# Kernel optimization log

Hardware: AMD Instinct MI355X
Metric: run time of the kernel (lower is better)

The kernel has to match this reference:

```python
import jax, jax.numpy as jnp
import numpy as np

E, T, A, H = 64, 128, 32, 4
S, O, QH1, QD, C1 = 256, 128, 128, 64, 128  # state, obs, query hidden, query/key dim, c hidden


def setup_inputs() -> dict:
    key = jax.random.key(0)
    ks = jax.random.split(key, 10)
    w = 0.02
    return {
        "q_values": jax.random.normal(ks[0], (E, T, A), jnp.float32),
        "states": jax.random.normal(ks[1], (E, T, S), jnp.float32),
        "individual_fs": jax.random.normal(ks[2], (E, T, A, O), jnp.float32),
        "Wq1": jax.random.normal(ks[3], (S, QH1), jnp.float32) * w,
        "bq1": jnp.zeros((QH1,), jnp.float32),
        "Wq2": jax.random.normal(ks[4], (QH1, QD), jnp.float32) * w,
        "bq2": jnp.zeros((QD,), jnp.float32),
        "Wk": jax.random.normal(ks[5], (H, O, QD), jnp.float32) * w,
        "bk": jnp.zeros((H, QD), jnp.float32),
        "Wc1": jax.random.normal(ks[6], (S, C1), jnp.float32) * w,
        "bc1": jnp.zeros((C1,), jnp.float32),
        "Wc2": jax.random.normal(ks[7], (C1, 1), jnp.float32) * w,
        "bc2": jnp.zeros((1,), jnp.float32),
    }


def reference(q_values, states, individual_fs, Wq1, bq1, Wq2, bq2, Wk, bk, Wc1, bc1, Wc2, bc2):
    e, t, a = q_values.shape
    s = states.reshape(-1, states.shape[-1])              # (B, S), B = E*T
    f = individual_fs.reshape(e * t, a, -1)               # (B, A, O)
    # query embedding of state: 2-layer MLP with ReLU
    emb_s = jnp.maximum(s @ Wq1 + bq1, 0.0) @ Wq2 + bq2   # (B, QD)
    # all-agents, all-heads key extraction in one batched einsum
    emb_u = jnp.einsum('bao,hok->bahk', f, Wk) + bk       # (B, A, H, QD)
    # query-key dot products per agent/head, then sum over heads
    Lambda_i = jnp.einsum('bk,bahk->bah', emb_s, emb_u).sum(axis=-1)  # (B, A)
    # state-dependent scalar bias
    c_value = jnp.maximum(s @ Wc1 + bc1, 0.0) @ Wc2 + bc2  # (B, 1)
    Q_tot = jnp.sum(Lambda_i * q_values.reshape(-1, a), axis=-1, keepdims=True) + c_value
    return Q_tot.reshape(e, t, 1)
```

## Files before the change

kernel.cpp:

```cpp
#include <hip/hip_runtime.h>


static constexpr int Sd  = 256;
static constexpr int Ad  = 32;
static constexpr int Od  = 128;
static constexpr int QDd = 64;

static constexpr size_t WS_WKT   = 0;
static constexpr size_t WS_BKSUM = 8192;
static constexpr size_t WS_M     = 8256;
static constexpr size_t WS_V0    = 24640;
static constexpr size_t WS_MBETA = 24768;
static constexpr size_t WS_BETA0 = 24896;
static constexpr size_t WS_BIAS  = 24960;
static constexpr size_t WS_V     = 33216;

__global__ void qatten_prep1(const float* __restrict__ Wk, const float* __restrict__ bk,
                             float* __restrict__ WkT, float* __restrict__ bkSum)
{
    int idx = blockIdx.x * 256 + threadIdx.x;
    int k = idx >> 7;
    int o = idx & 127;
    float s = 0.f;
#pragma unroll
    for (int h = 0; h < 4; ++h) s += Wk[h * (Od * QDd) + o * QDd + k];
    WkT[k * Od + o] = s;
    if (idx < QDd) {
        float t = 0.f;
#pragma unroll
        for (int h = 0; h < 4; ++h) t += bk[h * QDd + idx];
        bkSum[idx] = t;
    }
}

__global__ void qatten_prep2(const float* __restrict__ Wq2, const float* __restrict__ bq2,
                             const float* __restrict__ WkT, const float* __restrict__ bkSum,
                             float* __restrict__ M, float* __restrict__ v0,
                             float* __restrict__ m_beta, float* __restrict__ beta0)
{
    int idx = blockIdx.x * 256 + threadIdx.x;
    int j = idx >> 7;
    int o = idx & 127;
    float acc = 0.f;
    for (int k = 0; k < QDd; ++k)
        acc = fmaf(Wq2[j * QDd + k], WkT[k * Od + o], acc);
    M[j * Od + o] = acc;
    if (idx < 128) {
        float a = 0.f;
        for (int k = 0; k < QDd; ++k) a = fmaf(bq2[k], WkT[k * Od + idx], a);
        v0[idx] = a;
    } else if (idx < 256) {
        const int jj = idx - 128;
        float a = 0.f;
        for (int k = 0; k < QDd; ++k) a = fmaf(Wq2[jj * QDd + k], bkSum[k], a);
        m_beta[jj] = a;
    }
    if (idx == 0) {
        float a = 0.f;
        for (int k = 0; k < QDd; ++k) a = fmaf(bq2[k], bkSum[k], a);
        beta0[0] = a;
    }
}

static constexpr int NBM = 16;

__global__ __launch_bounds__(256, 4) void qatten_mlp(
    const float* __restrict__ qv, const float* __restrict__ st,
    const float* __restrict__ Wq1, const float* __restrict__ bq1,
    const float* __restrict__ Wc1, const float* __restrict__ bc1,
    const float* __restrict__ Wc2, const float* __restrict__ bc2,
    const float* __restrict__ M, const float* __restrict__ v0,
    const float* __restrict__ m_beta, const float* __restrict__ beta0p,
    float* __restrict__ v_ws, float* __restrict__ bias_ws)
{
    __shared__ float s_lds[NBM][Sd];
    __shared__ float h_lds[NBM][258];
    __shared__ float q_lds[NBM][Ad];

    const int tid = threadIdx.x;
    const int b0 = blockIdx.x * NBM;

    {
        const float4* sp = (const float4*)(st + (size_t)b0 * Sd);
        float4* sl = (float4*)&s_lds[0][0];
#pragma unroll
        for (int i = 0; i < 4; ++i) sl[tid + i * 256] = sp[tid + i * 256];
        float* ql = &q_lds[0][0];
#pragma unroll
        for (int i = 0; i < 2; ++i) ql[tid + i * 256] = qv[(size_t)b0 * Ad + tid + i * 256];
    }
    __syncthreads();

    {
        const float* W  = (tid < 128) ? (Wq1 + tid) : (Wc1 + (tid - 128));
        const float  bb = (tid < 128) ? bq1[tid] : bc1[tid - 128];
        float acc[NBM];
#pragma unroll
        for (int r = 0; r < NBM; ++r) acc[r] = 0.f;
        for (int i = 0; i < Sd; i += 4) {
            const float w0 = W[(size_t)(i + 0) * 128];
            const float w1 = W[(size_t)(i + 1) * 128];
            const float w2 = W[(size_t)(i + 2) * 128];
            const float w3 = W[(size_t)(i + 3) * 128];
#pragma unroll
            for (int r = 0; r < NBM; ++r) {
                const float4 sv = *(const float4*)&s_lds[r][i];
                float a = acc[r];
                a = fmaf(sv.x, w0, a);
                a = fmaf(sv.y, w1, a);
                a = fmaf(sv.z, w2, a);
                a = fmaf(sv.w, w3, a);
                acc[r] = a;
            }
        }
#pragma unroll
        for (int r = 0; r < NBM; ++r)
            h_lds[r][tid] = fmaxf(acc[r] + bb, 0.f);
    }
    __syncthreads();

    {
        const int o = tid & 127;
        const int rg = (tid >> 7) * 8;
        float acc[8];
#pragma unroll
        for (int r = 0; r < 8; ++r) acc[r] = 0.f;
        for (int j = 0; j < 128; j += 4) {
            const float m0 = M[(size_t)(j + 0) * 128 + o];
            const float m1 = M[(size_t)(j + 1) * 128 + o];
            const float m2 = M[(size_t)(j + 2) * 128 + o];
            const float m3 = M[(size_t)(j + 3) * 128 + o];
#pragma unroll
            for (int r = 0; r < 8; ++r) {
                const float4 hv = *(const float4*)&h_lds[rg + r][j];
                float a = acc[r];
                a = fmaf(hv.x, m0, a);
                a = fmaf(hv.y, m1, a);
                a = fmaf(hv.z, m2, a);
                a = fmaf(hv.w, m3, a);
                acc[r] = a;
            }
        }
        const float v0o = v0[o];
#pragma unroll
        for (int r = 0; r < 8; ++r)
            v_ws[(size_t)(b0 + rg + r) * 128 + o] = acc[r] + v0o;
    }

    {
        const int b = tid >> 4;
        const int i = tid & 15;
        float pb = 0.f, pc = 0.f;
#pragma unroll
        for (int t = 0; t < 8; ++t) {
            const int j = i + 16 * t;
            pb = fmaf(h_lds[b][j], m_beta[j], pb);
            pc = fmaf(h_lds[b][128 + j], Wc2[j], pc);
        }
        float pq = q_lds[b][i] + q_lds[b][i + 16];
#pragma unroll
        for (int d = 8; d >= 1; d >>= 1) {
            pb += __shfl_down(pb, d, 16);
            pc += __shfl_down(pc, d, 16);
            pq += __shfl_down(pq, d, 16);
        }
        if (i == 0) bias_ws[b0 + b] = (pc + bc2[0]) + (pb + beta0p[0]) * pq;
    }
}

__global__ __launch_bounds__(256, 8) void qatten_stream(
    const float* __restrict__ qv, const float* __restrict__ fs,
    const float* __restrict__ v_ws, const float* __restrict__ bias_ws,
    float* __restrict__ out)
{
    const int gw   = (blockIdx.x * 256 + threadIdx.x) >> 6;
    const int lane = threadIdx.x & 63;
    const int oq   = lane & 31;
    const int a0   = lane >> 5;

    const float4* fb = (const float4*)(fs + (size_t)gw * (Ad * Od));
    const float4  v4 = *(const float4*)(v_ws + (size_t)gw * Od + oq * 4);
    const float*  qb = qv + (size_t)gw * Ad;

    float s = 0.f;
#pragma unroll
    for (int r = 0; r < 16; ++r) {
        const int a = a0 + 2 * r;
        const float4 f4 = fb[a * 32 + oq];
        float d = f4.x * v4.x;
        d = fmaf(f4.y, v4.y, d);
        d = fmaf(f4.z, v4.z, d);
        d = fmaf(f4.w, v4.w, d);
        s = fmaf(qb[a], d, s);
    }
#pragma unroll
    for (int d = 32; d >= 1; d >>= 1) s += __shfl_xor(s, d);
    if (lane == 0) out[gw] = s + bias_ws[gw];
}

extern "C" void kernel_launch(void* const* d_in, const int* in_sizes, int n_in,
                              void* d_out, int out_size, void* d_ws, size_t ws_size,
                              hipStream_t stream) {
    const float* qv  = (const float*)d_in[0];
    const float* st  = (const float*)d_in[1];
    const float* fs  = (const float*)d_in[2];
    const float* Wq1 = (const float*)d_in[3];
    const float* bq1 = (const float*)d_in[4];
    const float* Wq2 = (const float*)d_in[5];
    const float* bq2 = (const float*)d_in[6];
    const float* Wk  = (const float*)d_in[7];
    const float* bk  = (const float*)d_in[8];
    const float* Wc1 = (const float*)d_in[9];
    const float* bc1 = (const float*)d_in[10];
    const float* Wc2 = (const float*)d_in[11];
    const float* bc2 = (const float*)d_in[12];
    float* out = (float*)d_out;

    float* ws      = (float*)d_ws;
    float* WkT     = ws + WS_WKT;
    float* bkSum   = ws + WS_BKSUM;
    float* Mm      = ws + WS_M;
    float* v0      = ws + WS_V0;
    float* m_beta  = ws + WS_MBETA;
    float* beta0   = ws + WS_BETA0;
    float* bias_ws = ws + WS_BIAS;
    float* v_ws    = ws + WS_V;

    qatten_prep1<<<32, 256, 0, stream>>>(Wk, bk, WkT, bkSum);
    qatten_prep2<<<64, 256, 0, stream>>>(Wq2, bq2, WkT, bkSum, Mm, v0, m_beta, beta0);
    qatten_mlp<<<512, 256, 0, stream>>>(qv, st, Wq1, bq1, Wc1, bc1, Wc2, bc2,
                                        Mm, v0, m_beta, beta0, v_ws, bias_ws);
    qatten_stream<<<2048, 256, 0, stream>>>(qv, fs, v_ws, bias_ws, out);
}
```

Baseline: 268.7 us.

## Fuse MLP and feature-stream kernels with register prefetch of individual_fs

Merges the per-row MLP kernel and the streaming dot-product kernel into one kernel handling 8 rows per block, so the intermediate v and bias stay in LDS instead of a global workspace. The first 6 rows' individual_fs tiles are prefetched into registers before and during the MLP stages to overlap the dominant 33MB read with compute. It also replaces __syncthreads with a custom LDS-only waitcnt barrier. In exchange, row batching drops from 16 to 8, so weights are re-read twice as often, and the many prefetch registers may reduce occupancy.

```diff
diff --git a/kernel.cpp b/kernel.cpp
--- a/kernel.cpp
+++ b/kernel.cpp
@@ -5,6 +5,7 @@
 static constexpr int Ad  = 32;
 static constexpr int Od  = 128;
 static constexpr int QDd = 64;
+static constexpr int NB  = 8;
 
 static constexpr size_t WS_WKT   = 0;
 static constexpr size_t WS_BKSUM = 8192;
@@ -12,8 +13,13 @@
 static constexpr size_t WS_V0    = 24640;
 static constexpr size_t WS_MBETA = 24768;
 static constexpr size_t WS_BETA0 = 24896;
-static constexpr size_t WS_BIAS  = 24960;
-static constexpr size_t WS_V     = 33216;
+
+__device__ __forceinline__ void barrier_lds() {
+    asm volatile("" ::: "memory");
+    __builtin_amdgcn_s_waitcnt(0xc07f);
+    __builtin_amdgcn_s_barrier();
+    asm volatile("" ::: "memory");
+}
 
 __global__ void qatten_prep1(const float* __restrict__ Wk, const float* __restrict__ bk,
                              float* __restrict__ WkT, float* __restrict__ bkSum)
@@ -62,76 +68,88 @@
     }
 }
 
-static constexpr int NBM = 16;
-
-__global__ __launch_bounds__(256, 4) void qatten_mlp(
-    const float* __restrict__ qv, const float* __restrict__ st,
+__global__ __launch_bounds__(256, 4) void qatten_fused(
+    const float* __restrict__ qv, const float* __restrict__ st, const float* __restrict__ fs,
     const float* __restrict__ Wq1, const float* __restrict__ bq1,
     const float* __restrict__ Wc1, const float* __restrict__ bc1,
     const float* __restrict__ Wc2, const float* __restrict__ bc2,
     const float* __restrict__ M, const float* __restrict__ v0,
     const float* __restrict__ m_beta, const float* __restrict__ beta0p,
-    float* __restrict__ v_ws, float* __restrict__ bias_ws)
+    float* __restrict__ out)
 {
-    __shared__ float s_lds[NBM][Sd];
-    __shared__ float h_lds[NBM][258];
-    __shared__ float q_lds[NBM][Ad];
+    __shared__ float s_lds[NB][Sd];
+    __shared__ float h_lds[NB][258];
+    __shared__ float v_lds[NB][Od];
+    __shared__ float q_lds[NB][Ad];
+    __shared__ float red_lds[NB][4];
+    __shared__ float bias_lds[NB];
 
     const int tid = threadIdx.x;
-    const int b0 = blockIdx.x * NBM;
-
-    {
-        const float4* sp = (const float4*)(st + (size_t)b0 * Sd);
-        float4* sl = (float4*)&s_lds[0][0];
-#pragma unroll
-        for (int i = 0; i < 4; ++i) sl[tid + i * 256] = sp[tid + i * 256];
-        float* ql = &q_lds[0][0];
-#pragma unroll
-        for (int i = 0; i < 2; ++i) ql[tid + i * 256] = qv[(size_t)b0 * Ad + tid + i * 256];
-    }
-    __syncthreads();
+    const int b0 = blockIdx.x * NB;
+    const int oq = tid & 31;
+    const int ag = tid >> 5;
+
+    const float4* sp = (const float4*)(st + (size_t)b0 * Sd);
+    const float4 sstage0 = sp[tid];
+    const float4 sstage1 = sp[tid + 256];
+    const float  qstage  = qv[(size_t)b0 * Ad + tid];
+
+    const float4* fbase = (const float4*)(fs + (size_t)b0 * (Ad * Od));
+    float4 pf[16];
+#pragma unroll
+    for (int b = 0; b < 4; ++b)
+#pragma unroll
+        for (int r = 0; r < 4; ++r)
+            pf[b * 4 + r] = fbase[(size_t)b * 1024 + (ag + 8 * r) * 32 + oq];
+
+    ((float4*)&s_lds[0][0])[tid]       = sstage0;
+    ((float4*)&s_lds[0][0])[tid + 256] = sstage1;
+    (&q_lds[0][0])[tid] = qstage;
+    barrier_lds();
 
     {
         const float* W  = (tid < 128) ? (Wq1 + tid) : (Wc1 + (tid - 128));
         const float  bb = (tid < 128) ? bq1[tid] : bc1[tid - 128];
-        float acc[NBM];
-#pragma unroll
-        for (int r = 0; r < NBM; ++r) acc[r] = 0.f;
-        for (int i = 0; i < Sd; i += 4) {
-            const float w0 = W[(size_t)(i + 0) * 128];
-            const float w1 = W[(size_t)(i + 1) * 128];
-            const float w2 = W[(size_t)(i + 2) * 128];
-            const float w3 = W[(size_t)(i + 3) * 128];
-#pragma unroll
-            for (int r = 0; r < NBM; ++r) {
-                const float4 sv = *(const float4*)&s_lds[r][i];
+        float acc[NB];
+#pragma unroll
+        for (int r = 0; r < NB; ++r) acc[r] = 0.f;
+        for (int i = 0; i < Sd; i += 8) {
+            float w[8];
+#pragma unroll
+            for (int u = 0; u < 8; ++u) w[u] = W[(size_t)(i + u) * 128];
+#pragma unroll
+            for (int r = 0; r < NB; ++r) {
+                const float4 s0 = *(const float4*)&s_lds[r][i];
+                const float4 s1 = *(const float4*)&s_lds[r][i + 4];
                 float a = acc[r];
-                a = fmaf(sv.x, w0, a);
-                a = fmaf(sv.y, w1, a);
-                a = fmaf(sv.z, w2, a);
-                a = fmaf(sv.w, w3, a);
+                a = fmaf(s0.x, w[0], a);
+                a = fmaf(s0.y, w[1], a);
+                a = fmaf(s0.z, w[2], a);
+                a = fmaf(s0.w, w[3], a);
+                a = fmaf(s1.x, w[4], a);
+                a = fmaf(s1.y, w[5], a);
+                a = fmaf(s1.z, w[6], a);
+                a = fmaf(s1.w, w[7], a);
                 acc[r] = a;
             }
         }
 #pragma unroll
-        for (int r = 0; r < NBM; ++r)
+        for (int r = 0; r < NB; ++r)
             h_lds[r][tid] = fmaxf(acc[r] + bb, 0.f);
     }
-    __syncthreads();
+    barrier_lds();
 
     {
         const int o = tid & 127;
-        const int rg = (tid >> 7) * 8;
-        float acc[8];
-#pragma unroll
-        for (int r = 0; r < 8; ++r) acc[r] = 0.f;
+        const int rg = (tid >> 7) * 4;
+        float acc[4] = {0.f, 0.f, 0.f, 0.f};
         for (int j = 0; j < 128; j += 4) {
             const float m0 = M[(size_t)(j + 0) * 128 + o];
             const float m1 = M[(size_t)(j + 1) * 128 + o];
             const float m2 = M[(size_t)(j + 2) * 128 + o];
             const float m3 = M[(size_t)(j + 3) * 128 + o];
 #pragma unroll
-            for (int r = 0; r < 8; ++r) {
+            for (int r = 0; r < 4; ++r) {
                 const float4 hv = *(const float4*)&h_lds[rg + r][j];
                 float a = acc[r];
                 a = fmaf(hv.x, m0, a);
@@ -143,59 +161,105 @@
         }
         const float v0o = v0[o];
 #pragma unroll
-        for (int r = 0; r < 8; ++r)
-            v_ws[(size_t)(b0 + rg + r) * 128 + o] = acc[r] + v0o;
-    }
-
-    {
-        const int b = tid >> 4;
-        const int i = tid & 15;
+        for (int r = 0; r < 4; ++r) v_lds[rg + r][o] = acc[r] + v0o;
+    }
+
+    float4 pf2[8];
+#pragma unroll
+    for (int b = 0; b < 2; ++b)
+#pragma unroll
+        for (int r = 0; r < 4; ++r)
+            pf2[b * 4 + r] = fbase[(size_t)(4 + b) * 1024 + (ag + 8 * r) * 32 + oq];
+
+    {
+        const int b = tid >> 5;
+        const int i = tid & 31;
         float pb = 0.f, pc = 0.f;
 #pragma unroll
-        for (int t = 0; t < 8; ++t) {
-            const int j = i + 16 * t;
+        for (int t = 0; t < 4; ++t) {
+            const int j = i + 32 * t;
             pb = fmaf(h_lds[b][j], m_beta[j], pb);
             pc = fmaf(h_lds[b][128 + j], Wc2[j], pc);
         }
-        float pq = q_lds[b][i] + q_lds[b][i + 16];
-#pragma unroll
-        for (int d = 8; d >= 1; d >>= 1) {
-            pb += __shfl_down(pb, d, 16);
-            pc += __shfl_down(pc, d, 16);
-            pq += __shfl_down(pq, d, 16);
-        }
-        if (i == 0) bias_ws[b0 + b] = (pc + bc2[0]) + (pb + beta0p[0]) * pq;
-    }
-}
-
-__global__ __launch_bounds__(256, 8) void qatten_stream(
-    const float* __restrict__ qv, const float* __restrict__ fs,
-    const float* __restrict__ v_ws, const float* __restrict__ bias_ws,
-    float* __restrict__ out)
-{
-    const int gw   = (blockIdx.x * 256 + threadIdx.x) >> 6;
-    const int lane = threadIdx.x & 63;
-    const int oq   = lane & 31;
-    const int a0   = lane >> 5;
-
-    const float4* fb = (const float4*)(fs + (size_t)gw * (Ad * Od));
-    const float4  v4 = *(const float4*)(v_ws + (size_t)gw * Od + oq * 4);
-    const float*  qb = qv + (size_t)gw * Ad;
-
-    float s = 0.f;
-#pragma unroll
-    for (int r = 0; r < 16; ++r) {
-        const int a = a0 + 2 * r;
-        const float4 f4 = fb[a * 32 + oq];
-        float d = f4.x * v4.x;
-        d = fmaf(f4.y, v4.y, d);
-        d = fmaf(f4.z, v4.z, d);
-        d = fmaf(f4.w, v4.w, d);
-        s = fmaf(qb[a], d, s);
-    }
-#pragma unroll
-    for (int d = 32; d >= 1; d >>= 1) s += __shfl_xor(s, d);
-    if (lane == 0) out[gw] = s + bias_ws[gw];
+        float pq = q_lds[b][i];
+#pragma unroll
+        for (int d = 16; d >= 1; d >>= 1) {
+            pb += __shfl_down(pb, d, 32);
+            pc += __shfl_down(pc, d, 32);
+            pq += __shfl_down(pq, d, 32);
+        }
+        if (i == 0) bias_lds[b] = (pc + bc2[0]) + (pb + beta0p[0]) * pq;
+    }
+    barrier_lds();
+
+    {
+        float accb[NB];
+#pragma unroll
+        for (int b = 0; b < 4; ++b) {
+            const float4 v4 = *(const float4*)&v_lds[b][oq * 4];
+            float s = 0.f;
+#pragma unroll
+            for (int r = 0; r < 4; ++r) {
+                const float4 f4 = pf[b * 4 + r];
+                float d = f4.x * v4.x;
+                d = fmaf(f4.y, v4.y, d);
+                d = fmaf(f4.z, v4.z, d);
+                d = fmaf(f4.w, v4.w, d);
+                s = fmaf(q_lds[b][ag + 8 * r], d, s);
+            }
+            accb[b] = s;
+        }
+#pragma unroll
+        for (int b = 0; b < 2; ++b) {
+            const float4 v4 = *(const float4*)&v_lds[4 + b][oq * 4];
+            float s = 0.f;
+#pragma unroll
+            for (int r = 0; r < 4; ++r) {
+                const float4 f4 = pf2[b * 4 + r];
+                float d = f4.x * v4.x;
+                d = fmaf(f4.y, v4.y, d);
+                d = fmaf(f4.z, v4.z, d);
+                d = fmaf(f4.w, v4.w, d);
+                s = fmaf(q_lds[4 + b][ag + 8 * r], d, s);
+            }
+            accb[4 + b] = s;
+        }
+#pragma unroll
+        for (int b = 6; b < 8; ++b) {
+            const float4 v4 = *(const float4*)&v_lds[b][oq * 4];
+            const float4* fb = fbase + (size_t)b * 1024;
+            float s = 0.f;
+#pragma unroll
+            for (int r = 0; r < 4; ++r) {
+                const float4 f4 = fb[(ag + 8 * r) * 32 + oq];
+                float d = f4.x * v4.x;
+                d = fmaf(f4.y, v4.y, d);
+                d = fmaf(f4.z, v4.z, d);
+                d = fmaf(f4.w, v4.w, d);
+                s = fmaf(q_lds[b][ag + 8 * r], d, s);
+            }
+            accb[b] = s;
+        }
+        const int lane = tid & 63;
+        const int wv = tid >> 6;
+#pragma unroll
+        for (int b = 0; b < NB; ++b) {
+            float s = accb[b];
+#pragma unroll
+            for (int d = 32; d >= 1; d >>= 1) s += __shfl_xor(s, d);
+            accb[b] = s;
+        }
+        if (lane == 0) {
+#pragma unroll
+            for (int b = 0; b < NB; ++b) red_lds[b][wv] = accb[b];
+        }
+    }
+    barrier_lds();
+
+    if (tid < NB) {
+        out[b0 + tid] = red_lds[tid][0] + red_lds[tid][1] +
+                        red_lds[tid][2] + red_lds[tid][3] + bias_lds[tid];
+    }
 }
 
 extern "C" void kernel_launch(void* const* d_in, const int* in_sizes, int n_in,
@@ -216,19 +280,17 @@
     const float* bc2 = (const float*)d_in[12];
     float* out = (float*)d_out;
 
-    float* ws      = (float*)d_ws;
-    float* WkT     = ws + WS_WKT;
-    float* bkSum   = ws + WS_BKSUM;
-    float* Mm      = ws + WS_M;
-    float* v0      = ws + WS_V0;
-    float* m_beta  = ws + WS_MBETA;
-    float* beta0   = ws + WS_BETA0;
-    float* bias_ws = ws + WS_BIAS;
-    float* v_ws    = ws + WS_V;
+    float* ws     = (float*)d_ws;
+    float* WkT    = ws + WS_WKT;
+    float* bkSum  = ws + WS_BKSUM;
+    float* Mm     = ws + WS_M;
+    float* v0     = ws + WS_V0;
+    float* m_beta = ws + WS_MBETA;
+    float* beta0  = ws + WS_BETA0;
+    (void)ws_size; (void)in_sizes; (void)n_in; (void)out_size;
 
     qatten_prep1<<<32, 256, 0, stream>>>(Wk, bk, WkT, bkSum);
     qatten_prep2<<<64, 256, 0, stream>>>(Wq2, bq2, WkT, bkSum, Mm, v0, m_beta, beta0);
-    qatten_mlp<<<512, 256, 0, stream>>>(qv, st, Wq1, bq1, Wc1, bc1, Wc2, bc2,
-                                        Mm, v0, m_beta, beta0, v_ws, bias_ws);
-    qatten_stream<<<2048, 256, 0, stream>>>(qv, fs, v_ws, bias_ws, out);
-}
+    qatten_fused<<<1024, 256, 0, stream>>>(qv, st, fs, Wq1, bq1, Wc1, bc1,
+                                           Wc2, bc2, Mm, v0, m_beta, beta0, out);
+}
```

Result: faster. 260.4 us (-3.1%).
